# Kernel tuning notes

Hardware: AMD Instinct MI355X
Metric: run time of the kernel (lower is better)

## Reference

```python
import jax, jax.numpy as jnp
import numpy as np

N = 20000; E = 160000; C = 64; SH = 9; NB = 8
S_DIM = 16; MS_HID = 64; FC_HID = 64
RATE = 0.1; LAMBDA = 0.5; R_MAX = 5.0; EV_PER = 16
K = int(RATE * N)          # static master-node count (top-k selection)
E_V = EV_PER * K           # static virtual-edge budget


def _safe_len(vec):
    # smooth norm, safe under autodiff at zero-length edges (self loops)
    return jnp.sqrt(jnp.sum(vec * vec, axis=-1, keepdims=True) + 1e-12)


def _sh(vec):
    # real spherical harmonics lmax=2, 'component' normalization, on unit vectors
    n = vec / _safe_len(vec)
    x, y, z = n[:, 0], n[:, 1], n[:, 2]
    s3 = jnp.sqrt(3.0); s15 = jnp.sqrt(15.0); s5 = jnp.sqrt(5.0)
    return jnp.stack([
        jnp.ones_like(x),
        s3 * x, s3 * y, s3 * z,
        s15 * x * y, s15 * y * z, 0.5 * s5 * (3 * z * z - 1.0),
        s15 * x * z, 0.5 * s15 * (x * x - y * y),
    ], axis=-1)  # [E, 9]


def _bessel(r):
    # Bessel radial basis with p=6 polynomial cutoff envelope; r: [E,1]
    n = jnp.arange(1, NB + 1, dtype=r.dtype)
    b = jnp.sqrt(2.0 / R_MAX) * jnp.sin(n * jnp.pi * r / R_MAX) / jnp.clip(r, 1e-9)
    u = jnp.clip(r / R_MAX, 0.0, 1.0); p = 6.0
    env = 1.0 - (p + 1) * (p + 2) / 2 * u ** p + p * (p + 2) * u ** (p + 1) - p * (p + 1) / 2 * u ** (p + 2)
    return b * env  # [E, NB]


def _conv(h, src, dst, sh, ef, emask, n_nodes, fc_w1, fc_b1, fc_w2, fc_b2, lin_w):
    # TFN-style tensor-product conv: per-edge weights from radial MLP,
    # message = flatten(h[dst] outer sh) * w -> linear -> scatter-mean to src
    w = jax.nn.relu(ef @ fc_w1 + fc_b1) @ fc_w2 + fc_b2            # [E, C*SH]
    tp = (h[dst][:, :, None] * sh[:, None, :]).reshape(sh.shape[0], -1) * w
    msg = (tp @ lin_w) * emask[:, None]                            # [E, C]
    agg = jax.ops.segment_sum(msg, src, num_segments=n_nodes)
    deg = jax.ops.segment_sum(emask, src, num_segments=n_nodes)
    return agg / jnp.clip(deg, 1.0)[:, None]


def setup_inputs() -> dict:
    key = jax.random.key(0)
    ks = jax.random.split(key, 12)
    def lin(k, i, o):
        return (jax.random.normal(k, (i, o), jnp.float32) / np.sqrt(i)).astype(jnp.float32)
    return {
        "h": jax.random.normal(ks[0], (N, C), jnp.float32),
        "pos": jax.random.uniform(ks[1], (N, 3), jnp.float32) * 10.0,
        "edge_index": jax.random.randint(ks[2], (2, E), 0, N, dtype=jnp.int32),
        "fc_w1": lin(ks[3], NB, FC_HID), "fc_b1": jnp.zeros((FC_HID,), jnp.float32),
        "fc_w2": lin(ks[4], FC_HID, C * SH), "fc_b2": jnp.zeros((C * SH,), jnp.float32),
        "lin_w": lin(ks[5], C * SH, C),
        "ms_w1": lin(ks[6], S_DIM, MS_HID), "ms_b1": jnp.zeros((MS_HID,), jnp.float32),
        "ms_w2": lin(ks[7], MS_HID, 1), "ms_b2": jnp.zeros((1,), jnp.float32),
        "vg_wq": lin(ks[8], S_DIM, S_DIM), "vg_wk": lin(ks[9], S_DIM, S_DIM),
    }


def reference(h, pos, fc_w1, fc_b1, fc_w2, fc_b2, lin_w,
              ms_w1, ms_b1, ms_w2, ms_b2, vg_wq, vg_wk, edge_index):
    src, dst = edge_index[0], edge_index[1]
    vec = pos[src] - pos[dst]
    sh = _sh(vec)
    ef = _bessel(_safe_len(vec))
    ones_e = jnp.ones((E,), h.dtype)
    h_update = _conv(h, src, dst, sh, ef, ones_e, N, fc_w1, fc_b1, fc_w2, fc_b2, lin_w)
    h_local = h_update + h  # in_dim == out_dim -> pad is a no-op

    # --- master selection (top-k by learned score; static K) ---
    h_sc = h_local[:, :S_DIM]
    score = jax.nn.sigmoid(
        (jax.nn.relu(h_sc @ ms_w1 + ms_b1) @ ms_w2 + ms_b2).squeeze(-1))  # [N]
    _, top_idx = jax.lax.top_k(score, K)
    node_mask = jnp.zeros((N,), h.dtype).at[top_idx].set(1.0)
    m = score * node_mask
    master_idx = jnp.sort(top_idx)

    # relabel full-graph ids -> master-subgraph ids (masked subgraph extraction)
    node2m = jnp.full((N,), -1, jnp.int32).at[master_idx].set(jnp.arange(K, dtype=jnp.int32))
    src_m, dst_m = node2m[src], node2m[dst]
    e_mask = ((src_m >= 0) & (dst_m >= 0)).astype(h.dtype)
    src_mc = jnp.where(src_m >= 0, src_m, 0)
    dst_mc = jnp.where(dst_m >= 0, dst_m, 0)
    adj = jnp.zeros((K, K), h.dtype).at[src_mc, dst_mc].add(e_mask)

    h_master = h_local[master_idx]
    pos_master = pos[master_idx]
    h_ms = h_master[:, :S_DIM]

    # --- virtual edge generation (attention, thresholded by lambda) ---
    q = h_ms @ vg_wq; kk = h_ms @ vg_wk
    attn = jax.nn.sigmoid(q @ kk.T / np.sqrt(S_DIM))  # [K, K]
    exist = (adj > 0) | jnp.eye(K, dtype=bool)
    A_virtual = jnp.where((~exist) & (attn > LAMBDA), 1.0, 0.0).astype(h.dtype)
    vvals, vidx = jax.lax.top_k((attn * A_virtual).reshape(-1), E_V)
    v_src = (vidx // K).astype(jnp.int32); v_dst = (vidx % K).astype(jnp.int32)
    v_mask = (vvals > 0).astype(h.dtype)

    src_all = jnp.concatenate([src_mc, v_src])
    dst_all = jnp.concatenate([dst_mc, v_dst])
    mask_all = jnp.concatenate([e_mask, v_mask])
    vec_m = pos_master[src_all] - pos_master[dst_all]
    sh_m = _sh(vec_m)
    ef_m = _bessel(_safe_len(vec_m))
    h_m_update = _conv(h_master, src_all, dst_all, sh_m, ef_m, mask_all, K,
                       fc_w1, fc_b1, fc_w2, fc_b2, lin_w)
    h_hier = h_m_update + h_master

    h_hier_exp = jnp.zeros_like(h_local).at[master_idx].set(h_hier)
    m_e = m[:, None]
    h_final = (1.0 - m_e) * h_local + m_e * h_hier_exp
    return (h_final, pos, A_virtual, m)
```

## Files before the change

kernel.cpp:

```cpp
#include <hip/hip_runtime.h>
#include <stdint.h>

constexpr int N_   = 20000;
constexpr int E_   = 160000;
constexpr int C_   = 64;
constexpr int K_   = 2000;
constexpr int EV_  = 32000;
constexpr int EALL_ = E_ + EV_;
constexpr int CSH_ = 576;
constexpr int TB_  = 64;

constexpr size_t OFF_AGG    = 0;
constexpr size_t OFF_DEG    = 5120000;
constexpr size_t OFF_AGGM   = 5200000;
constexpr size_t OFF_DEGM   = 5712000;
constexpr size_t OFF_RANK   = 5720000;
constexpr size_t OFF_MASKA  = 5800000;
constexpr size_t OFF_EXIST  = 6568000;
constexpr size_t OFF_HIST   = 10568000;
constexpr size_t OFF_STATE  = 10572096;
constexpr size_t ZERO_BYTES = 10572352;
constexpr size_t OFF_HLOCAL = 10572352;
constexpr size_t OFF_KEY    = 15692352;
constexpr size_t OFF_SCORE  = 15852352;
constexpr size_t OFF_N2M    = 15932352;
constexpr size_t OFF_MIDX   = 16012352;
constexpr size_t OFF_HM     = 16020352;
constexpr size_t OFF_POSM   = 16532352;
constexpr size_t OFF_Q      = 16556352;
constexpr size_t OFF_KBUF   = 16684352;
constexpr size_t OFF_SRCA   = 16812352;
constexpr size_t OFF_DSTA   = 17580352;
constexpr size_t OFF_TMAX   = 18348352;
constexpr size_t OFF_CAND   = 18410880;

struct RState {
    unsigned long long prefix;
    int R;
    unsigned int cand_count;
    unsigned int sel_count;
    int bin_thresh;
    unsigned int total;
    unsigned int pad;
};

__global__ void k_w0(const float* __restrict__ fc_b1, const float* __restrict__ fc_w2,
                     const float* __restrict__ fc_b2, int* __restrict__ w0nz)
{
    __shared__ float hid0[64];
    __shared__ int nz;
    int tid = threadIdx.x;
    if (tid == 0) nz = 0;
    if (tid < 64) hid0[tid] = fmaxf(fc_b1[tid], 0.0f);
    __syncthreads();
    if (tid < CSH_) {
        float acc = fc_b2[tid];
        for (int k = 0; k < 64; k++) acc += hid0[k] * fc_w2[k * CSH_ + tid];
        if (acc != 0.0f) atomicOr(&nz, 1);
    }
    __syncthreads();
    if (tid == 0) *w0nz = nz;
}

__global__ __launch_bounds__(256) void k_prep(
    int n_edges, const int* __restrict__ src, const int* __restrict__ dst,
    const float* __restrict__ mask, const float* __restrict__ posn,
    const int* __restrict__ w0nz, float* __restrict__ deg,
    float* __restrict__ edata, unsigned int* __restrict__ cnt)
{
    int e = blockIdx.x * 256 + threadIdx.x;
    bool valid = e < n_edges;
    int s_i = 0, d_i = 0; float msk = 0.0f;
    if (valid) {
        msk = mask ? mask[e] : 1.0f;
        if (msk != 0.0f) { s_i = src[e]; d_i = dst[e]; }
    }
    bool active = valid && (msk != 0.0f);

    float vx = 0.f, vy = 0.f, vz = 0.f;
    if (active) {
        vx = posn[s_i*3+0] - posn[d_i*3+0];
        vy = posn[s_i*3+1] - posn[d_i*3+1];
        vz = posn[s_i*3+2] - posn[d_i*3+2];
    }
    float r = sqrtf(vx*vx + vy*vy + vz*vz + 1e-12f);
    float invr = 1.0f / r;
    float x = vx*invr, y = vy*invr, z = vz*invr;
    const float s3 = 1.7320508075688772f, s15 = 3.872983346207417f, s5 = 2.23606797749979f;
    float sh[9];
    sh[0] = 1.0f; sh[1] = s3*x; sh[2] = s3*y; sh[3] = s3*z;
    sh[4] = s15*x*y; sh[5] = s15*y*z; sh[6] = 0.5f*s5*(3.0f*z*z - 1.0f);
    sh[7] = s15*x*z; sh[8] = 0.5f*s15*(x*x - y*y);

    float u = r * 0.2f; u = u > 1.0f ? 1.0f : u;
    float u2 = u*u, u6 = u2*u2*u2, u7 = u6*u, u8 = u7*u;
    float env = 1.0f - 28.0f*u6 + 48.0f*u7 - 21.0f*u8;
    float rc = r > 1e-9f ? r : 1e-9f;
    const float bpref = 0.6324555320336759f;
    const float PIov5 = 0.6283185307179586f;
    float ef[8];
    #pragma unroll
    for (int n = 0; n < 8; n++)
        ef[n] = bpref * sinf(PIov5 * r * (float)(n + 1)) / rc * env;

    if (active) atomicAdd(&deg[s_i], msk);

    bool contrib = active && !((env == 0.0f) && (*w0nz == 0));
    int lane = threadIdx.x & 63;
    unsigned long long b = __ballot(contrib);
    int wc = __popcll(b);
    int base = 0;
    if (lane == 0 && wc) base = (int)atomicAdd(cnt, (unsigned)wc);
    base = __shfl(base, 0);
    if (contrib) {
        int slot = base + __popcll(b & ((1ull << lane) - 1ull));
        float* p = edata + (size_t)slot * 20;
        #pragma unroll
        for (int n = 0; n < 8; n++) p[n] = ef[n];
        #pragma unroll
        for (int t = 0; t < 9; t++) p[8+t] = sh[t];
        p[17] = __int_as_float(s_i);
        p[18] = __int_as_float(d_i);
        p[19] = msk;
    }
}

__global__ __launch_bounds__(256, 3) void k_convg(
    const unsigned int* __restrict__ cnt, const float* __restrict__ edata,
    const float* __restrict__ hn,
    const float* __restrict__ fc_w1, const float* __restrict__ fc_b1,
    const float* __restrict__ fc_w2, const float* __restrict__ fc_b2,
    const float* __restrict__ lin_w, float* __restrict__ agg)
{
    __shared__ float s_misc[TB_ * 12];
    __shared__ __align__(16) float s_hid[64 * 64];
    __shared__ __align__(16) float s_tp[64 * 68];
    __shared__ __align__(16) float s_w[4096];

    const int tid = threadIdx.x;
    const int oq = (tid & 15) * 4;
    const int e0 = (tid >> 4) * 4;

    const int nheavy = (int)*cnt;
    const int nblk = (nheavy + TB_ - 1) / TB_;

    for (int blk = blockIdx.x; blk < nblk; blk += gridDim.x) {
        const int ebase = blk * TB_;
        int nE = nheavy - ebase; if (nE > TB_) nE = TB_;

        __syncthreads();
        for (int idx = tid; idx < TB_ * 12; idx += 256) {
            int e = idx / 12, f = idx - 12 * e;
            float v = 0.0f;
            if (e < nE) {
                const float* p = edata + (size_t)(ebase + e) * 20;
                v = (f < 9) ? p[8 + f] : (f == 9) ? p[17] : (f == 10) ? p[19] : p[18];
            }
            s_misc[idx] = v;
        }
        for (int idx = tid; idx < TB_ * 64; idx += 256) {
            int k = idx >> 6, e = idx & 63;
            float hv = 0.0f;
            if (e < nE) {
                const float* p = edata + (size_t)(ebase + e) * 20;
                float acc = fc_b1[k];
                #pragma unroll
                for (int n = 0; n < 8; n++) acc += p[n] * fc_w1[n * 64 + k];
                hv = fmaxf(acc, 0.0f);
            }
            s_hid[k * 64 + e] = hv;
        }
        float acc[4][4] = {{0,0,0,0},{0,0,0,0},{0,0,0,0},{0,0,0,0}};
        __syncthreads();

        const int d0 = __float_as_int(s_misc[(e0+0) * 12 + 11]);
        const int d1 = __float_as_int(s_misc[(e0+1) * 12 + 11]);
        const int d2 = __float_as_int(s_misc[(e0+2) * 12 + 11]);
        const int d3 = __float_as_int(s_misc[(e0+3) * 12 + 11]);

        for (int cj = 0; cj < 9; cj++) {
            const int j0 = cj * 64;
            if (cj) __syncthreads();
            for (int i4 = tid; i4 < 1024; i4 += 256) {
                int k = i4 >> 4, q4 = (i4 & 15) * 4;
                *reinterpret_cast<float4*>(&s_w[k * 64 + q4]) =
                    *reinterpret_cast<const float4*>(&fc_w2[k * CSH_ + j0 + q4]);
            }
            __syncthreads();

            const int jb = j0 + oq;
            const int c0 = jb / 9, c1 = (jb + 3) / 9;
            float hA0 = hn[d0 * 64 + c0], hB0 = hn[d0 * 64 + c1];
            float hA1 = hn[d1 * 64 + c0], hB1 = hn[d1 * 64 + c1];
            float hA2 = hn[d2 * 64 + c0], hB2 = hn[d2 * 64 + c1];
            float hA3 = hn[d3 * 64 + c0], hB3 = hn[d3 * 64 + c1];

            float a[4][4];
            #pragma unroll
            for (int q = 0; q < 4; q++) {
                float b = fc_b2[jb + q];
                a[0][q]=b; a[1][q]=b; a[2][q]=b; a[3][q]=b;
            }
            #pragma unroll 4
            for (int k = 0; k < 64; k++) {
                float4 w4 = *reinterpret_cast<const float4*>(&s_w[k * 64 + oq]);
                float4 h4 = *reinterpret_cast<const float4*>(&s_hid[k * 64 + e0]);
                a[0][0]+=h4.x*w4.x; a[0][1]+=h4.x*w4.y; a[0][2]+=h4.x*w4.z; a[0][3]+=h4.x*w4.w;
                a[1][0]+=h4.y*w4.x; a[1][1]+=h4.y*w4.y; a[1][2]+=h4.y*w4.z; a[1][3]+=h4.y*w4.w;
                a[2][0]+=h4.z*w4.x; a[2][1]+=h4.z*w4.y; a[2][2]+=h4.z*w4.z; a[2][3]+=h4.z*w4.w;
                a[3][0]+=h4.w*w4.x; a[3][1]+=h4.w*w4.y; a[3][2]+=h4.w*w4.z; a[3][3]+=h4.w*w4.w;
            }
            #pragma unroll
            for (int q = 0; q < 4; q++) {
                int j = jb + q; int cc = j / 9; int si = j - 9 * cc;
                float4 tpv;
                tpv.x = (cc == c0 ? hA0 : hB0) * s_misc[(e0+0) * 12 + si] * a[0][q];
                tpv.y = (cc == c0 ? hA1 : hB1) * s_misc[(e0+1) * 12 + si] * a[1][q];
                tpv.z = (cc == c0 ? hA2 : hB2) * s_misc[(e0+2) * 12 + si] * a[2][q];
                tpv.w = (cc == c0 ? hA3 : hB3) * s_misc[(e0+3) * 12 + si] * a[3][q];
                *reinterpret_cast<float4*>(&s_tp[(oq + q) * 68 + e0]) = tpv;
            }
            __syncthreads();

            for (int i4 = tid; i4 < 1024; i4 += 256) {
                *reinterpret_cast<float4*>(&s_w[i4 * 4]) =
                    *reinterpret_cast<const float4*>(&lin_w[j0 * 64 + i4 * 4]);
            }
            __syncthreads();

            #pragma unroll 4
            for (int jj = 0; jj < 64; jj++) {
                float4 l4 = *reinterpret_cast<const float4*>(&s_w[jj * 64 + oq]);
                float4 t4 = *reinterpret_cast<const float4*>(&s_tp[jj * 68 + e0]);
                acc[0][0]+=t4.x*l4.x; acc[0][1]+=t4.x*l4.y; acc[0][2]+=t4.x*l4.z; acc[0][3]+=t4.x*l4.w;
                acc[1][0]+=t4.y*l4.x; acc[1][1]+=t4.y*l4.y; acc[1][2]+=t4.y*l4.z; acc[1][3]+=t4.y*l4.w;
                acc[2][0]+=t4.z*l4.x; acc[2][1]+=t4.z*l4.y; acc[2][2]+=t4.z*l4.z; acc[2][3]+=t4.z*l4.w;
                acc[3][0]+=t4.w*l4.x; acc[3][1]+=t4.w*l4.y; acc[3][2]+=t4.w*l4.z; acc[3][3]+=t4.w*l4.w;
            }
        }

        #pragma unroll
        for (int t = 0; t < 4; t++) {
            float mk = s_misc[(e0+t) * 12 + 10];
            if (mk != 0.0f) {
                int s = __float_as_int(s_misc[(e0+t) * 12 + 9]);
                #pragma unroll
                for (int q = 0; q < 4; q++) atomicAdd(&agg[s * 64 + oq + q], acc[t][q] * mk);
            }
        }
    }
}

__global__ __launch_bounds__(256) void k_hlscore(const float* __restrict__ h,
    const float* __restrict__ agg, const float* __restrict__ deg,
    const float* __restrict__ ms_w1, const float* __restrict__ ms_b1,
    const float* __restrict__ ms_w2, const float* __restrict__ ms_b2,
    float* __restrict__ h_local, float* __restrict__ score, unsigned long long* __restrict__ key)
{
    int wid = threadIdx.x >> 6, lane = threadIdx.x & 63;
    int n = blockIdx.x * 4 + wid;
    if (n >= N_) return;
    float d = fmaxf(deg[n], 1.0f);
    float hl = h[n*64 + lane] + agg[n*64 + lane] / d;
    h_local[n*64 + lane] = hl;
    float acc = ms_b1[lane];
    #pragma unroll
    for (int i = 0; i < 16; i++) acc += __shfl(hl, i) * ms_w1[i*64 + lane];
    acc = fmaxf(acc, 0.0f);
    float part = acc * ms_w2[lane];
    #pragma unroll
    for (int off = 32; off > 0; off >>= 1) part += __shfl_xor(part, off);
    if (lane == 0) {
        float s = part + ms_b2[0];
        float sc = 1.0f / (1.0f + expf(-s));
        score[n] = sc;
        key[n] = ((unsigned long long)__float_as_uint(sc) << 32)
               | (unsigned long long)(0xFFFFFFFFu - (unsigned)n);
    }
}

__global__ __launch_bounds__(256) void k_rank(const unsigned long long* __restrict__ key,
                                              int* __restrict__ rankcnt)
{
    int i = blockIdx.x * 256 + threadIdx.x;
    int seg = blockIdx.y;
    int lo = seg * 1250, hi = lo + 1250;
    unsigned long long my = (i < N_) ? key[i] : ~0ull;
    int cnt = 0;
    #pragma unroll 8
    for (int j = lo; j < hi; j++) cnt += (key[j] > my) ? 1 : 0;
    if (i < N_ && cnt) atomicAdd(&rankcnt[i], cnt);
}

__global__ __launch_bounds__(1024) void k_scanfin(const int* __restrict__ rankcnt,
    const float* __restrict__ score, int* __restrict__ node2m, int* __restrict__ midx,
    float* __restrict__ m_out)
{
    __shared__ int wsum[16];
    __shared__ int wbase[16];
    __shared__ int s_base;
    int tid = threadIdx.x, lane = tid & 63, wv = tid >> 6;
    if (tid == 0) s_base = 0;
    __syncthreads();
    for (int c = 0; c < 20; c++) {
        int idx = c * 1024 + tid;
        int sel = 0;
        if (idx < N_) {
            sel = (rankcnt[idx] < K_) ? 1 : 0;
            m_out[idx] = sel ? score[idx] : 0.0f;
        }
        int v = sel;
        #pragma unroll
        for (int off = 1; off < 64; off <<= 1) {
            int u = __shfl_up(v, off);
            if (lane >= off) v += u;
        }
        if (lane == 63) wsum[wv] = v;
        __syncthreads();
        if (tid == 0) {
            int runb = s_base;
            for (int w = 0; w < 16; w++) { wbase[w] = runb; runb += wsum[w]; }
            s_base = runb;
        }
        __syncthreads();
        if (idx < N_) {
            if (sel) { int rk = wbase[wv] + v - 1; node2m[idx] = rk; midx[rk] = idx; }
            else node2m[idx] = -1;
        }
    }
}

__global__ __launch_bounds__(256) void k_mastex(const int* __restrict__ midx,
    const float* __restrict__ h_local, const float* __restrict__ pos,
    const float* __restrict__ vg_wq, const float* __restrict__ vg_wk,
    const int* __restrict__ src, const int* __restrict__ dst, const int* __restrict__ node2m,
    float* __restrict__ h_m, float* __restrict__ pos_m,
    float* __restrict__ qbuf, float* __restrict__ kbuf,
    int* __restrict__ src_all, int* __restrict__ dst_all,
    float* __restrict__ mask_all, unsigned char* __restrict__ exist)
{
    int b = blockIdx.x;
    if (b < 500) {
        int mi = b * 4 + (threadIdx.x >> 6);
        int lane = threadIdx.x & 63;
        int node = midx[mi];
        h_m[mi*64 + lane] = h_local[node*64 + lane];
        if (lane < 3) pos_m[mi*3 + lane] = pos[node*3 + lane];
        if (lane < 32) {
            int j = lane & 15;
            const float* wm = (lane < 16) ? vg_wq : vg_wk;
            float acc = 0.0f;
            #pragma unroll
            for (int i = 0; i < 16; i++) acc += h_local[node*64 + i] * wm[i*16 + j];
            if (lane < 16) qbuf[mi*16 + j] = acc; else kbuf[mi*16 + j] = acc;
        }
    } else {
        int e = (b - 500) * 256 + threadIdx.x;
        int sm = node2m[src[e]], dm = node2m[dst[e]];
        bool em = (sm >= 0) && (dm >= 0);
        int smc = sm >= 0 ? sm : 0;
        int dmc = dm >= 0 ? dm : 0;
        src_all[e] = smc; dst_all[e] = dmc; mask_all[e] = em ? 1.0f : 0.0f;
        if (em) exist[smc * K_ + dmc] = 1;
    }
}

constexpr int NTILE_ = (K_ / 16) * (K_ / 16);
__global__ __launch_bounds__(256) void k_attn1(const float* __restrict__ qbuf,
    const float* __restrict__ kbuf, const unsigned char* __restrict__ exist,
    float* __restrict__ Av, float* __restrict__ tmax, unsigned int* __restrict__ hist,
    RState* st, unsigned int* __restrict__ done_ctr)
{
    constexpr int TBK = K_ / 16;
    __shared__ float sq[16][17], sk[16][17];
    __shared__ unsigned int lh[1024];
    __shared__ float wmax[4];
    __shared__ unsigned int ha[1024], hb[1024];
    __shared__ unsigned int s_last;
    int tid = threadIdx.x;
    for (int b = tid; b < 1024; b += 256) lh[b] = 0;

    for (int t = blockIdx.x; t < NTILE_; t += gridDim.x) {
        int bi = t / TBK, bj = t % TBK;
        int i0 = bi * 16, j0 = bj * 16;
        int r = tid >> 4, c = tid & 15;
        __syncthreads();
        sq[r][c] = qbuf[(i0 + r) * 16 + c];
        sk[r][c] = kbuf[(j0 + r) * 16 + c];
        __syncthreads();
        int ti = tid >> 4, tj = tid & 15;
        float dot = 0.0f;
        #pragma unroll
        for (int cc = 0; cc < 16; cc++) dot += sq[ti][cc] * sk[tj][cc];
        float attn = 1.0f / (1.0f + expf(-dot * 0.25f));
        int gi = i0 + ti, gj = j0 + tj;
        int flat = gi * K_ + gj;
        bool ex = (exist[flat] != 0) || (gi == gj);
        bool av = (!ex) && (attn > 0.5f);
        Av[flat] = av ? 1.0f : 0.0f;
        float cv = av ? attn : 0.0f;
        if (av) {
            unsigned bin = (__float_as_uint(attn) - 0x3F000000u) >> 13;
            if (bin > 1023u) bin = 1023u;
            atomicAdd(&lh[bin], 1u);
        }
        float wm = cv;
        #pragma unroll
        for (int off = 32; off > 0; off >>= 1) wm = fmaxf(wm, __shfl_xor(wm, off));
        int wid = tid >> 6, lane = tid & 63;
        if (lane == 0) wmax[wid] = wm;
        __syncthreads();
        if (tid == 0) tmax[t] = fmaxf(fmaxf(wmax[0], wmax[1]), fmaxf(wmax[2], wmax[3]));
    }
    __syncthreads();
    for (int b = tid; b < 1024; b += 256) {
        unsigned v = lh[b];
        if (v) atomicAdd(&hist[b], v);
    }
    __syncthreads();
    __threadfence();
    if (tid == 0) s_last = (atomicAdd(done_ctr, 1u) == (unsigned)gridDim.x - 1u) ? 1u : 0u;
    __syncthreads();
    if (!s_last) return;
    __threadfence();
    for (int b = tid; b < 1024; b += 256) ha[b] = hist[b];
    __syncthreads();
    unsigned* srcp = ha; unsigned* dstp = hb;
    for (int off = 1; off < 1024; off <<= 1) {
        for (int b = tid; b < 1024; b += 256)
            dstp[b] = srcp[b] + ((b + off < 1024) ? srcp[b + off] : 0u);
        __syncthreads();
        unsigned* tmp = srcp; srcp = dstp; dstp = tmp;
    }
    unsigned total = srcp[0];
    int R = (total < (unsigned)EV_) ? (int)total : EV_;
    if (tid == 0) {
        st->R = R; st->total = total; st->cand_count = 0; st->sel_count = 0;
        if (R == 0) st->bin_thresh = 1024;
    }
    __syncthreads();
    if (R > 0) {
        for (int b = tid; b < 1024; b += 256) {
            unsigned hi2 = (b == 1023) ? 0u : srcp[b + 1];
            if ((int)srcp[b] >= R && (int)hi2 < R) st->bin_thresh = b;
        }
    }
}

__global__ __launch_bounds__(256) void k_attn2(const float* __restrict__ qbuf,
    const float* __restrict__ kbuf, const unsigned char* __restrict__ exist,
    const float* __restrict__ tmax, RState* st, unsigned long long* __restrict__ cand)
{
    constexpr int TBK = K_ / 16;
    __shared__ float sq[16][17], sk[16][17];
    __shared__ int wb[4];
    __shared__ int bb;
    int tid = threadIdx.x;
    unsigned tbits = 0x3F000000u + ((unsigned)st->bin_thresh << 13);

    for (int t = blockIdx.x; t < NTILE_; t += gridDim.x) {
        if (__float_as_uint(tmax[t]) < tbits) continue;
        int bi = t / TBK, bj = t % TBK;
        int i0 = bi * 16, j0 = bj * 16;
        int r = tid >> 4, c = tid & 15;
        __syncthreads();
        sq[r][c] = qbuf[(i0 + r) * 16 + c];
        sk[r][c] = kbuf[(j0 + r) * 16 + c];
        __syncthreads();
        int ti = tid >> 4, tj = tid & 15;
        float dot = 0.0f;
        #pragma unroll
        for (int cc = 0; cc < 16; cc++) dot += sq[ti][cc] * sk[tj][cc];
        float attn = 1.0f / (1.0f + expf(-dot * 0.25f));
        int gi = i0 + ti, gj = j0 + tj;
        int flat = gi * K_ + gj;
        bool ex = (exist[flat] != 0) || (gi == gj);
        bool store = (!ex) && (attn > 0.5f) && (__float_as_uint(attn) >= tbits);

        unsigned long long keyv = ((unsigned long long)__float_as_uint(attn) << 32)
                                | (unsigned long long)(0xFFFFFFFFu - (unsigned)flat);
        int wid = tid >> 6, lane = tid & 63;
        unsigned long long b = __ballot(store);
        int wc = __popcll(b);
        if (lane == 0) wb[wid] = wc;
        __syncthreads();
        if (tid == 0) {
            int s = 0;
            for (int w = 0; w < 4; w++) { int cc2 = wb[w]; wb[w] = s; s += cc2; }
            bb = s ? (int)atomicAdd(&st->cand_count, (unsigned)s) : 0;
        }
        __syncthreads();
        if (store) {
            int slot = bb + wb[wid] + __popcll(b & ((1ull << lane) - 1ull));
            cand[slot] = keyv;
        }
    }
}

__global__ __launch_bounds__(1024) void k_radixsel(RState* st,
    const unsigned long long* __restrict__ cand,
    int* __restrict__ src_all, int* __restrict__ dst_all, float* __restrict__ mask_all)
{
    __shared__ unsigned int lh[256];
    __shared__ unsigned int suf[256];
    __shared__ unsigned int s_tie[8192];
    __shared__ unsigned int s_pref, s_R, s_tiecnt, s_cfth;
    int tid = threadIdx.x;
    int n = (int)st->cand_count;
    int R = st->R;
    if (tid == 0) { s_pref = 0x3F000000u; s_R = (unsigned)R; s_tiecnt = 0; s_cfth = 0; }
    __syncthreads();

    unsigned long long T;
    if (R > 0) {
        for (int p = 0; p < 3; p++) {
            if (tid < 256) lh[tid] = 0;
            __syncthreads();
            unsigned pref = s_pref;
            int sh_d = 16 - 8 * p;
            unsigned pm = 0xFFFFFFFFu << (sh_d + 8);
            for (int i = tid; i < n; i += 1024) {
                unsigned a = (unsigned)(cand[i] >> 32);
                if ((a & pm) == (pref & pm))
                    atomicAdd(&lh[(a >> sh_d) & 255u], 1u);
            }
            __syncthreads();
            if (tid < 256) suf[tid] = lh[tid];
            __syncthreads();
            for (int off = 1; off < 256; off <<= 1) {
                unsigned v = 0;
                if (tid < 256 && tid + off < 256) v = suf[tid + off];
                __syncthreads();
                if (tid < 256) suf[tid] += v;
                __syncthreads();
            }
            if (tid < 256) {
                unsigned Rc = s_R;
                unsigned hi2 = (tid == 255) ? 0u : suf[tid + 1];
                if (suf[tid] >= Rc && hi2 < Rc) {
                    s_pref = pref | ((unsigned)tid << sh_d);
                    s_R = Rc - hi2;
                }
            }
            __syncthreads();
        }
        unsigned Ta = s_pref;
        unsigned Rrem = s_R;
        for (int i = tid; i < n; i += 1024) {
            unsigned long long kv = cand[i];
            if ((unsigned)(kv >> 32) == Ta) {
                unsigned pos = atomicAdd(&s_tiecnt, 1u);
                if (pos < 8192u) s_tie[pos] = (unsigned)(kv & 0xFFFFFFFFull);
            }
        }
        __syncthreads();
        unsigned Cq = s_tiecnt; if (Cq > 8192u) Cq = 8192u;
        if (Rrem >= 1u && Rrem < Cq) {
            for (int i = tid; i < (int)Cq; i += 1024) {
                unsigned me = s_tie[i];
                unsigned r = 0;
                for (int j = 0; j < (int)Cq; j++) r += (s_tie[j] > me) ? 1u : 0u;
                if (r == Rrem - 1u) s_cfth = me;
            }
        }
        __syncthreads();
        T = ((unsigned long long)Ta << 32) | (unsigned long long)s_cfth;
    } else {
        T = ~0ull;
    }

    int lane = tid & 63;
    for (int i0 = 0; i0 < n; i0 += 1024) {
        int i = i0 + tid;
        bool sel = (i < n) && (cand[i] >= T);
        unsigned long long b = __ballot(sel);
        int wc = __popcll(b);
        int basep = 0;
        if (lane == 0 && wc) basep = (int)atomicAdd(&st->sel_count, (unsigned)wc);
        basep = __shfl(basep, 0);
        if (sel) {
            int slot = basep + __popcll(b & ((1ull << lane) - 1ull));
            if (slot < EV_) {
                unsigned flat = 0xFFFFFFFFu - (unsigned)(cand[i] & 0xFFFFFFFFull);
                src_all[E_ + slot] = (int)(flat / (unsigned)K_);
                dst_all[E_ + slot] = (int)(flat % (unsigned)K_);
                mask_all[E_ + slot] = 1.0f;
            }
        }
    }
}

__global__ void k_finalpos(const float* __restrict__ h_local, const int* __restrict__ node2m,
    const float* __restrict__ aggm, const float* __restrict__ degm, const float* __restrict__ h_m,
    const float* __restrict__ m_out, const float* __restrict__ pos,
    float* __restrict__ out_h, float* __restrict__ out_pos)
{
    int idx = blockIdx.x * 256 + threadIdx.x;
    if (idx < N_ * 3) out_pos[idx] = pos[idx];
    if (idx >= N_ * C_) return;
    int i = idx >> 6, c = idx & 63;
    float mval = m_out[i];
    int mi = node2m[i];
    float hh = 0.0f;
    if (mi >= 0) hh = aggm[mi*64 + c] / fmaxf(degm[mi], 1.0f) + h_m[mi*64 + c];
    out_h[idx] = (1.0f - mval) * h_local[idx] + mval * hh;
}

extern "C" void kernel_launch(void* const* d_in, const int* in_sizes, int n_in,
                              void* d_out, int out_size, void* d_ws, size_t ws_size,
                              hipStream_t stream)
{
    (void)in_sizes; (void)n_in; (void)out_size; (void)ws_size;
    const float* h     = (const float*)d_in[0];
    const float* pos   = (const float*)d_in[1];
    const int*   eidx  = (const int*)d_in[2];
    const float* fc_w1 = (const float*)d_in[3];
    const float* fc_b1 = (const float*)d_in[4];
    const float* fc_w2 = (const float*)d_in[5];
    const float* fc_b2 = (const float*)d_in[6];
    const float* lin_w = (const float*)d_in[7];
    const float* ms_w1 = (const float*)d_in[8];
    const float* ms_b1 = (const float*)d_in[9];
    const float* ms_w2 = (const float*)d_in[10];
    const float* ms_b2 = (const float*)d_in[11];
    const float* vg_wq = (const float*)d_in[12];
    const float* vg_wk = (const float*)d_in[13];

    char* ws = (char*)d_ws;
    float* agg     = (float*)(ws + OFF_AGG);
    float* deg     = (float*)(ws + OFF_DEG);
    float* aggm    = (float*)(ws + OFF_AGGM);
    float* degm    = (float*)(ws + OFF_DEGM);
    int*   rankcnt = (int*)(ws + OFF_RANK);
    float* mask_all = (float*)(ws + OFF_MASKA);
    unsigned char* exist = (unsigned char*)(ws + OFF_EXIST);
    unsigned int* hist = (unsigned int*)(ws + OFF_HIST);
    RState* st     = (RState*)(ws + OFF_STATE);
    unsigned int* cnt0 = (unsigned int*)(ws + OFF_STATE + 64);
    unsigned int* cnt1 = (unsigned int*)(ws + OFF_STATE + 68);
    int*   w0nz    = (int*)(ws + OFF_STATE + 72);
    unsigned int* done_a1 = (unsigned int*)(ws + OFF_STATE + 76);
    float* h_local = (float*)(ws + OFF_HLOCAL);
    unsigned long long* key = (unsigned long long*)(ws + OFF_KEY);
    float* score   = (float*)(ws + OFF_SCORE);
    int*   node2m  = (int*)(ws + OFF_N2M);
    int*   midx    = (int*)(ws + OFF_MIDX);
    float* h_m     = (float*)(ws + OFF_HM);
    float* pos_m   = (float*)(ws + OFF_POSM);
    float* qbuf    = (float*)(ws + OFF_Q);
    float* kbuf    = (float*)(ws + OFF_KBUF);
    int*   src_all = (int*)(ws + OFF_SRCA);
    int*   dst_all = (int*)(ws + OFF_DSTA);
    float* tmax    = (float*)(ws + OFF_TMAX);
    unsigned long long* cand = (unsigned long long*)(ws + OFF_CAND);
    float* edata   = (float*)(ws + OFF_CAND);

    float* out_h   = (float*)d_out;
    float* out_pos = out_h + (size_t)N_ * C_;
    float* out_av  = out_pos + (size_t)N_ * 3;
    float* out_m   = out_av + (size_t)K_ * K_;

    hipMemsetAsync(ws, 0, ZERO_BYTES, stream);

    k_w0<<<1, 576, 0, stream>>>(fc_b1, fc_w2, fc_b2, w0nz);

    k_prep<<<E_ / 256, 256, 0, stream>>>(E_, eidx, eidx + E_, nullptr, pos, w0nz, deg, edata, cnt0);
    k_convg<<<768, 256, 0, stream>>>(cnt0, edata, h, fc_w1, fc_b1, fc_w2, fc_b2, lin_w, agg);

    k_hlscore<<<(N_ + 3) / 4, 256, 0, stream>>>(h, agg, deg, ms_w1, ms_b1, ms_w2, ms_b2,
                                                h_local, score, key);

    k_rank<<<dim3((N_ + 255) / 256, 16), 256, 0, stream>>>(key, rankcnt);
    k_scanfin<<<1, 1024, 0, stream>>>(rankcnt, score, node2m, midx, out_m);

    k_mastex<<<500 + E_ / 256, 256, 0, stream>>>(midx, h_local, pos, vg_wq, vg_wk,
        eidx, eidx + E_, node2m, h_m, pos_m, qbuf, kbuf, src_all, dst_all, mask_all, exist);

    k_attn1<<<1024, 256, 0, stream>>>(qbuf, kbuf, exist, out_av, tmax, hist, st, done_a1);
    k_attn2<<<1024, 256, 0, stream>>>(qbuf, kbuf, exist, tmax, st, cand);
    k_radixsel<<<1, 1024, 0, stream>>>(st, cand, src_all, dst_all, mask_all);

    k_prep<<<EALL_ / 256, 256, 0, stream>>>(EALL_, src_all, dst_all, mask_all, pos_m, w0nz,
                                            degm, edata, cnt1);
    k_convg<<<768, 256, 0, stream>>>(cnt1, edata, h_m, fc_w1, fc_b1, fc_w2, fc_b2, lin_w, aggm);

    k_finalpos<<<(N_ * C_ + 255) / 256, 256, 0, stream>>>(h_local, node2m, aggm, degm, h_m,
                                                          out_m, pos, out_h, out_pos);
}
```

Baseline: 737.8 us.

## Flatten attention kernels to row-major indexing and fuse memset into init kernel

```diff
diff --git a/kernel.cpp b/kernel.cpp
--- a/kernel.cpp
+++ b/kernel.cpp
@@ -9,6 +9,7 @@
 constexpr int EALL_ = E_ + EV_;
 constexpr int CSH_ = 576;
 constexpr int TB_  = 64;
+constexpr int NFLAT_ = K_ * K_;
 
 constexpr size_t OFF_AGG    = 0;
 constexpr size_t OFF_DEG    = 5120000;
@@ -19,7 +20,6 @@
 constexpr size_t OFF_EXIST  = 6568000;
 constexpr size_t OFF_HIST   = 10568000;
 constexpr size_t OFF_STATE  = 10572096;
-constexpr size_t ZERO_BYTES = 10572352;
 constexpr size_t OFF_HLOCAL = 10572352;
 constexpr size_t OFF_KEY    = 15692352;
 constexpr size_t OFF_SCORE  = 15852352;
@@ -31,8 +31,8 @@
 constexpr size_t OFF_KBUF   = 16684352;
 constexpr size_t OFF_SRCA   = 16812352;
 constexpr size_t OFF_DSTA   = 17580352;
-constexpr size_t OFF_TMAX   = 18348352;
-constexpr size_t OFF_CAND   = 18410880;
+constexpr size_t OFF_WMAX   = 18348352;
+constexpr size_t OFF_CAND   = 18598400;
 
 struct RState {
     unsigned long long prefix;
@@ -44,22 +44,30 @@
     unsigned int pad;
 };
 
-__global__ void k_w0(const float* __restrict__ fc_b1, const float* __restrict__ fc_w2,
-                     const float* __restrict__ fc_b2, int* __restrict__ w0nz)
-{
-    __shared__ float hid0[64];
-    __shared__ int nz;
-    int tid = threadIdx.x;
-    if (tid == 0) nz = 0;
-    if (tid < 64) hid0[tid] = fmaxf(fc_b1[tid], 0.0f);
-    __syncthreads();
-    if (tid < CSH_) {
-        float acc = fc_b2[tid];
-        for (int k = 0; k < 64; k++) acc += hid0[k] * fc_w2[k * CSH_ + tid];
-        if (acc != 0.0f) atomicOr(&nz, 1);
-    }
-    __syncthreads();
-    if (tid == 0) *w0nz = nz;
+__global__ __launch_bounds__(256) void k_init(const float* __restrict__ fc_b1,
+    const float* __restrict__ fc_w2, const float* __restrict__ fc_b2, char* __restrict__ ws)
+{
+    float4 zero4 = make_float4(0.f, 0.f, 0.f, 0.f);
+    float4* z = (float4*)ws;
+    int nz4 = (int)(OFF_STATE / 16);
+    for (int i = blockIdx.x * 256 + threadIdx.x; i < nz4; i += gridDim.x * 256) z[i] = zero4;
+    if (blockIdx.x == gridDim.x - 1) {
+        __shared__ float hid0[64];
+        __shared__ int nz;
+        int t = threadIdx.x;
+        float4* zs = (float4*)(ws + OFF_STATE);
+        if (t < 16) zs[t] = zero4;
+        if (t == 0) nz = 0;
+        if (t < 64) hid0[t] = fmaxf(fc_b1[t], 0.0f);
+        __syncthreads();
+        for (int j = t; j < CSH_; j += 256) {
+            float acc = fc_b2[j];
+            for (int k = 0; k < 64; k++) acc += hid0[k] * fc_w2[k * CSH_ + j];
+            if (acc != 0.0f) atomicOr(&nz, 1);
+        }
+        __syncthreads();
+        if (t == 0) *(int*)(ws + OFF_STATE + 72) = nz;
+    }
 }
 
 __global__ __launch_bounds__(256) void k_prep(
@@ -365,36 +373,31 @@
     }
 }
 
-constexpr int NTILE_ = (K_ / 16) * (K_ / 16);
 __global__ __launch_bounds__(256) void k_attn1(const float* __restrict__ qbuf,
     const float* __restrict__ kbuf, const unsigned char* __restrict__ exist,
-    float* __restrict__ Av, float* __restrict__ tmax, unsigned int* __restrict__ hist,
+    float* __restrict__ Av, float* __restrict__ wmax, unsigned int* __restrict__ hist,
     RState* st, unsigned int* __restrict__ done_ctr)
 {
-    constexpr int TBK = K_ / 16;
-    __shared__ float sq[16][17], sk[16][17];
     __shared__ unsigned int lh[1024];
-    __shared__ float wmax[4];
     __shared__ unsigned int ha[1024], hb[1024];
     __shared__ unsigned int s_last;
-    int tid = threadIdx.x;
+    int tid = threadIdx.x, lane = tid & 63;
     for (int b = tid; b < 1024; b += 256) lh[b] = 0;
-
-    for (int t = blockIdx.x; t < NTILE_; t += gridDim.x) {
-        int bi = t / TBK, bj = t % TBK;
-        int i0 = bi * 16, j0 = bj * 16;
-        int r = tid >> 4, c = tid & 15;
-        __syncthreads();
-        sq[r][c] = qbuf[(i0 + r) * 16 + c];
-        sk[r][c] = kbuf[(j0 + r) * 16 + c];
-        __syncthreads();
-        int ti = tid >> 4, tj = tid & 15;
+    __syncthreads();
+
+    const int stride = gridDim.x * 256;
+    for (int flat = blockIdx.x * 256 + tid; flat < NFLAT_; flat += stride) {
+        int gi = flat / K_;
+        int gj = flat - gi * K_;
+        const float4* qp = reinterpret_cast<const float4*>(qbuf + gi * 16);
+        const float4* kp = reinterpret_cast<const float4*>(kbuf + gj * 16);
         float dot = 0.0f;
         #pragma unroll
-        for (int cc = 0; cc < 16; cc++) dot += sq[ti][cc] * sk[tj][cc];
+        for (int c4 = 0; c4 < 4; c4++) {
+            float4 q4 = qp[c4], k4 = kp[c4];
+            dot += q4.x*k4.x + q4.y*k4.y + q4.z*k4.z + q4.w*k4.w;
+        }
         float attn = 1.0f / (1.0f + expf(-dot * 0.25f));
-        int gi = i0 + ti, gj = j0 + tj;
-        int flat = gi * K_ + gj;
         bool ex = (exist[flat] != 0) || (gi == gj);
         bool av = (!ex) && (attn > 0.5f);
         Av[flat] = av ? 1.0f : 0.0f;
@@ -407,10 +410,7 @@
         float wm = cv;
         #pragma unroll
         for (int off = 32; off > 0; off >>= 1) wm = fmaxf(wm, __shfl_xor(wm, off));
-        int wid = tid >> 6, lane = tid & 63;
-        if (lane == 0) wmax[wid] = wm;
-        __syncthreads();
-        if (tid == 0) tmax[t] = fmaxf(fmaxf(wmax[0], wmax[1]), fmaxf(wmax[2], wmax[3]));
+        if (lane == 0) wmax[flat >> 6] = wm;
     }
     __syncthreads();
     for (int b = tid; b < 1024; b += 256) {
@@ -423,7 +423,7 @@
     __syncthreads();
     if (!s_last) return;
     __threadfence();
-    for (int b = tid; b < 1024; b += 256) ha[b] = hist[b];
+    for (int b = tid; b < 1024; b += 256) ha[b] = atomicAdd(&hist[b], 0u);
     __syncthreads();
     unsigned* srcp = ha; unsigned* dstp = hb;
     for (int off = 1; off < 1024; off <<= 1) {
@@ -449,40 +449,39 @@
 
 __global__ __launch_bounds__(256) void k_attn2(const float* __restrict__ qbuf,
     const float* __restrict__ kbuf, const unsigned char* __restrict__ exist,
-    const float* __restrict__ tmax, RState* st, unsigned long long* __restrict__ cand)
-{
-    constexpr int TBK = K_ / 16;
-    __shared__ float sq[16][17], sk[16][17];
+    const float* __restrict__ wmax, RState* st, unsigned long long* __restrict__ cand)
+{
     __shared__ int wb[4];
     __shared__ int bb;
-    int tid = threadIdx.x;
+    int tid = threadIdx.x, lane = tid & 63, wv = tid >> 6;
     unsigned tbits = 0x3F000000u + ((unsigned)st->bin_thresh << 13);
-
-    for (int t = blockIdx.x; t < NTILE_; t += gridDim.x) {
-        if (__float_as_uint(tmax[t]) < tbits) continue;
-        int bi = t / TBK, bj = t % TBK;
-        int i0 = bi * 16, j0 = bj * 16;
-        int r = tid >> 4, c = tid & 15;
-        __syncthreads();
-        sq[r][c] = qbuf[(i0 + r) * 16 + c];
-        sk[r][c] = kbuf[(j0 + r) * 16 + c];
-        __syncthreads();
-        int ti = tid >> 4, tj = tid & 15;
-        float dot = 0.0f;
-        #pragma unroll
-        for (int cc = 0; cc < 16; cc++) dot += sq[ti][cc] * sk[tj][cc];
-        float attn = 1.0f / (1.0f + expf(-dot * 0.25f));
-        int gi = i0 + ti, gj = j0 + tj;
-        int flat = gi * K_ + gj;
-        bool ex = (exist[flat] != 0) || (gi == gj);
-        bool store = (!ex) && (attn > 0.5f) && (__float_as_uint(attn) >= tbits);
-
-        unsigned long long keyv = ((unsigned long long)__float_as_uint(attn) << 32)
-                                | (unsigned long long)(0xFFFFFFFFu - (unsigned)flat);
-        int wid = tid >> 6, lane = tid & 63;
+    const int stride = gridDim.x * 256;
+
+    for (int base = blockIdx.x * 256; base < NFLAT_; base += stride) {
+        int flat = base + tid;
+        bool wactive = __float_as_uint(wmax[(base + wv * 64) >> 6]) >= tbits;
+        bool store = false;
+        unsigned long long keyv = 0ull;
+        if (wactive) {
+            int gi = flat / K_;
+            int gj = flat - gi * K_;
+            const float4* qp = reinterpret_cast<const float4*>(qbuf + gi * 16);
+            const float4* kp = reinterpret_cast<const float4*>(kbuf + gj * 16);
+            float dot = 0.0f;
+            #pragma unroll
+            for (int c4 = 0; c4 < 4; c4++) {
+                float4 q4 = qp[c4], k4 = kp[c4];
+                dot += q4.x*k4.x + q4.y*k4.y + q4.z*k4.z + q4.w*k4.w;
+            }
+            float attn = 1.0f / (1.0f + expf(-dot * 0.25f));
+            bool ex = (exist[flat] != 0) || (gi == gj);
+            store = (!ex) && (attn > 0.5f) && (__float_as_uint(attn) >= tbits);
+            keyv = ((unsigned long long)__float_as_uint(attn) << 32)
+                 | (unsigned long long)(0xFFFFFFFFu - (unsigned)flat);
+        }
         unsigned long long b = __ballot(store);
         int wc = __popcll(b);
-        if (lane == 0) wb[wid] = wc;
+        if (lane == 0) wb[wv] = wc;
         __syncthreads();
         if (tid == 0) {
             int s = 0;
@@ -491,9 +490,10 @@
         }
         __syncthreads();
         if (store) {
-            int slot = bb + wb[wid] + __popcll(b & ((1ull << lane) - 1ull));
+            int slot = bb + wb[wv] + __popcll(b & ((1ull << lane) - 1ull));
             cand[slot] = keyv;
         }
+        __syncthreads();
     }
 }
 
@@ -651,7 +651,7 @@
     float* kbuf    = (float*)(ws + OFF_KBUF);
     int*   src_all = (int*)(ws + OFF_SRCA);
     int*   dst_all = (int*)(ws + OFF_DSTA);
-    float* tmax    = (float*)(ws + OFF_TMAX);
+    float* wmax    = (float*)(ws + OFF_WMAX);
     unsigned long long* cand = (unsigned long long*)(ws + OFF_CAND);
     float* edata   = (float*)(ws + OFF_CAND);
 
@@ -660,9 +660,7 @@
     float* out_av  = out_pos + (size_t)N_ * 3;
     float* out_m   = out_av + (size_t)K_ * K_;
 
-    hipMemsetAsync(ws, 0, ZERO_BYTES, stream);
-
-    k_w0<<<1, 576, 0, stream>>>(fc_b1, fc_w2, fc_b2, w0nz);
+    k_init<<<768, 256, 0, stream>>>(fc_b1, fc_w2, fc_b2, ws);
 
     k_prep<<<E_ / 256, 256, 0, stream>>>(E_, eidx, eidx + E_, nullptr, pos, w0nz, deg, edata, cnt0);
     k_convg<<<768, 256, 0, stream>>>(cnt0, edata, h, fc_w1, fc_b1, fc_w2, fc_b2, lin_w, agg);
@@ -676,8 +674,8 @@
     k_mastex<<<500 + E_ / 256, 256, 0, stream>>>(midx, h_local, pos, vg_wq, vg_wk,
         eidx, eidx + E_, node2m, h_m, pos_m, qbuf, kbuf, src_all, dst_all, mask_all, exist);
 
-    k_attn1<<<1024, 256, 0, stream>>>(qbuf, kbuf, exist, out_av, tmax, hist, st, done_a1);
-    k_attn2<<<1024, 256, 0, stream>>>(qbuf, kbuf, exist, tmax, st, cand);
+    k_attn1<<<1024, 256, 0, stream>>>(qbuf, kbuf, exist, out_av, wmax, hist, st, done_a1);
+    k_attn2<<<1024, 256, 0, stream>>>(qbuf, kbuf, exist, wmax, st, cand);
     k_radixsel<<<1, 1024, 0, stream>>>(st, cand, src_all, dst_all, mask_all);
 
     k_prep<<<EALL_ / 256, 256, 0, stream>>>(EALL_, src_all, dst_all, mask_all, pos_m, w0nz,
```

After: 714.8 us (median of 2 runs). 3.1% less time.
